# Performance work log

Hardware: AMD Instinct MI355X
Metric: run time of the kernel (lower is better)

The kernel has to match this reference:

```python
import jax, jax.numpy as jnp
import numpy as np

HEADS, DIM_HEAD = 8, 96
DIM = HEADS * DIM_HEAD            # 768
DEPTH = 8
MEM_LAYERS = (4, 5)               # layers with KNN-retrieval attention
TOPK = 32                         # num_retrieved_memories
CLIP_LEN, PREFIX_LEN = 10, 10
NEG = -1e9


def layernorm(x, g, b):
    m = x.mean(-1, keepdims=True)
    v = ((x - m) ** 2).mean(-1, keepdims=True)
    return (x - m) * jax.lax.rsqrt(v + 1e-5) * g + b


def attention(x, wq_l, wkv_l, wo_l, mem_k=None, mem_v=None):
    # one-headed key/values (memorizing-transformers style), multi-head queries
    b, n, _ = x.shape
    q = (x @ wq_l).reshape(b, n, HEADS, DIM_HEAD).transpose(0, 2, 1, 3)  # [b,h,n,d]
    q = q * (DIM_HEAD ** -0.5)
    kv = x @ wkv_l                                   # [b,n,2d]
    k, v = kv[..., :DIM_HEAD], kv[..., DIM_HEAD:]    # [b,n,d] each
    sim = jnp.einsum('bhid,bjd->bhij', q, k)         # local scores
    causal = jnp.tril(jnp.ones((n, n), dtype=bool))
    sim = jnp.where(causal, sim, NEG)
    if mem_k is not None:
        # exact inner-product top-k retrieval from per-batch memory bank
        mem_sim = jnp.einsum('bhid,bmd->bhim', q, mem_k)      # [b,h,n,M]
        top_sim, top_idx = jax.lax.top_k(mem_sim, TOPK)       # [b,h,n,K]
        mem_v_sel = jnp.take_along_axis(
            mem_v[:, None, None], top_idx[..., None], axis=3)  # [b,h,n,K,d]
        attn = jax.nn.softmax(jnp.concatenate([top_sim, sim], axis=-1), axis=-1)
        mem_attn, loc_attn = attn[..., :TOPK], attn[..., TOPK:]
        out = (jnp.einsum('bhij,bhijd->bhid', mem_attn, mem_v_sel)
               + jnp.einsum('bhij,bjd->bhid', loc_attn, v))
    else:
        attn = jax.nn.softmax(sim, axis=-1)
        out = jnp.einsum('bhij,bjd->bhid', attn, v)
    out = out.transpose(0, 2, 1, 3).reshape(b, n, DIM)
    return out @ wo_l


def setup_inputs() -> dict:
    key = jax.random.key(0)
    ks = jax.random.split(key, 12)
    s = 0.02
    inp = {
        'x': jax.random.normal(ks[0], (16, 640), jnp.float32),
        'linear_w': jax.random.normal(ks[1], (640, CLIP_LEN * DIM), jnp.float32) * s,
        'linear_b': jnp.zeros((CLIP_LEN * DIM,), jnp.float32),
        'prefix_const': jax.random.normal(ks[2], (PREFIX_LEN, DIM), jnp.float32),
        'ln1_g': jnp.ones((DEPTH, DIM), jnp.float32),
        'ln1_b': jnp.zeros((DEPTH, DIM), jnp.float32),
        'wq': jax.random.normal(ks[3], (DEPTH, DIM, DIM), jnp.float32) * s,
        'wkv': jax.random.normal(ks[4], (DEPTH, DIM, 2 * DIM_HEAD), jnp.float32) * s,
        'wo': jax.random.normal(ks[5], (DEPTH, DIM, DIM), jnp.float32) * s,
        'ln2_g': jnp.ones((DEPTH, DIM), jnp.float32),
        'ln2_b': jnp.zeros((DEPTH, DIM), jnp.float32),
        'w1': jax.random.normal(ks[6], (DEPTH, DIM, 4 * DIM), jnp.float32) * s,
        'b1': jnp.zeros((DEPTH, 4 * DIM), jnp.float32),
        'w2': jax.random.normal(ks[7], (DEPTH, 4 * DIM, DIM), jnp.float32) * s,
        'b2': jnp.zeros((DEPTH, DIM), jnp.float32),
        'lnf_g': jnp.ones((DIM,), jnp.float32),
        'lnf_b': jnp.zeros((DIM,), jnp.float32),
        'mem_k': jax.random.normal(ks[8], (16, 32768, DIM_HEAD), jnp.float32),
        'mem_v': jax.random.normal(ks[9], (16, 32768, DIM_HEAD), jnp.float32),
    }
    return inp


def reference(x, linear_w, linear_b, prefix_const,
              ln1_g, ln1_b, wq, wkv, wo, ln2_g, ln2_b,
              w1, b1, w2, b2, lnf_g, lnf_b, mem_k, mem_v):
    b = x.shape[0]
    # linear projection of clip feature -> clip_length tokens
    h = (x @ linear_w + linear_b).reshape(b, CLIP_LEN, DIM)
    prefix = jnp.broadcast_to(prefix_const[None], (b, PREFIX_LEN, DIM))
    t = jnp.concatenate([h, prefix], axis=1)  # [b, 20, dim]
    for l in range(DEPTH):
        mk, mv = (mem_k, mem_v) if l in MEM_LAYERS else (None, None)
        t = t + attention(layernorm(t, ln1_g[l], ln1_b[l]), wq[l], wkv[l], wo[l], mk, mv)
        hf = layernorm(t, ln2_g[l], ln2_b[l])
        t = t + (jax.nn.gelu(hf @ w1[l] + b1[l]) @ w2[l] + b2[l])
    t = layernorm(t, lnf_g, lnf_b)
    return t[:, CLIP_LEN:]  # [b, prefix_length, dim]
```

## Files before the change

### kernel.cpp

```cpp
#include <hip/hip_runtime.h>
#include <hip/hip_bf16.h>

#define BB 16
#define NSEQ 20
#define HEADS 8
#define DH 96
#define DIM 768
#define FF 3072
#define KMEM 32768
#define NCHUNK 4
#define CHUNK 8192
#define CAP 128
#define ALDS 776

typedef unsigned short u16;
typedef __attribute__((ext_vector_type(8))) short short8v;
typedef __attribute__((ext_vector_type(4))) float f32x4;

__device__ __forceinline__ u16 f2bu(float x) {
    __hip_bfloat16 h = __float2bfloat16(x);
    return *reinterpret_cast<u16*>(&h);
}

__global__ __launch_bounds__(256) void conv_k(const float* __restrict__ src, u16* __restrict__ dst, int n)
{
    int i = blockIdx.x * 256 + threadIdx.x;
    if (i < n) dst[i] = f2bu(src[i]);
}

__device__ __forceinline__ void tconv_tile(const float* __restrict__ src, u16* __restrict__ dst,
                                           int K, int N, int kt, int nt, int tx, int ty)
{
    __shared__ float tile[32][33];
    int k0 = kt * 32, n0 = nt * 32;
#pragma unroll
    for (int i = 0; i < 4; i++)
        tile[ty + 8 * i][tx] = src[(size_t)(k0 + ty + 8 * i) * N + n0 + tx];
    __syncthreads();
#pragma unroll
    for (int i = 0; i < 4; i++)
        dst[(size_t)(n0 + ty + 8 * i) * K + k0 + tx] = f2bu(tile[tx][ty + 8 * i]);
}

__global__ __launch_bounds__(256) void tconv_k(const float* __restrict__ src, u16* __restrict__ dst, int K, int N)
{
    int tilesN = N >> 5;
    tconv_tile(src, dst, K, N, blockIdx.x / tilesN, blockIdx.x % tilesN,
               threadIdx.x & 31, threadIdx.x >> 5);
}

__global__ __launch_bounds__(256) void wconv5L_k(const float* __restrict__ wq, const float* __restrict__ wkv,
    const float* __restrict__ wo, const float* __restrict__ w1, const float* __restrict__ w2,
    u16* __restrict__ wt, size_t wtStride)
{
    int l = blockIdx.y;
    wq += (size_t)l * 589824;
    wkv += (size_t)l * 147456;
    wo += (size_t)l * 589824;
    w1 += (size_t)l * 2359296;
    w2 += (size_t)l * 2359296;
    wt += (size_t)l * wtStride;
    int bx = blockIdx.x;
    int tx = threadIdx.x & 31, ty = threadIdx.x >> 5;
    if (bx < 576)       tconv_tile(wq,  wt + 0,       768, 768,  bx / 24,          bx % 24,          tx, ty);
    else if (bx < 720)  tconv_tile(wkv, wt + 589824,  768, 192,  (bx - 576) / 6,   (bx - 576) % 6,   tx, ty);
    else if (bx < 1296) tconv_tile(wo,  wt + 737280,  768, 768,  (bx - 720) / 24,  (bx - 720) % 24,  tx, ty);
    else if (bx < 3600) tconv_tile(w1,  wt + 1327104, 768, 3072, (bx - 1296) / 96, (bx - 1296) % 96, tx, ty);
    else                tconv_tile(w2,  wt + 3686400, 3072, 768, (bx - 3600) / 24, (bx - 3600) % 24, tx, ty);
}

__device__ __forceinline__ void storeC(float* C, size_t idx, float v) { C[idx] = v; }
__device__ __forceinline__ void storeC(u16* C, size_t idx, float v)   { C[idx] = f2bu(v); }

template <typename CT>
__global__ __launch_bounds__(256) void gemm_bt(const u16* __restrict__ A, const u16* __restrict__ Bt,
    const float* __restrict__ bias, const float* __restrict__ resid, CT* __restrict__ C,
    int M, int N, int K, int lda, int ldc, float scale, int act)
{
    int tid = threadIdx.x;
    int w = tid >> 6, lane = tid & 63;
    int m0 = blockIdx.y * 16;
    int n0 = blockIdx.x * 128 + w * 32;
    int row = lane & 15;
    int kg  = lane >> 4;
    const u16* arow = A + (size_t)(m0 + row) * lda + kg * 8;
    int c0 = n0 + row;
    int c1 = n0 + 16 + row;
    const u16* bt0 = Bt + (size_t)min(c0, N - 1) * K + kg * 8;
    const u16* bt1 = Bt + (size_t)min(c1, N - 1) * K + kg * 8;
    f32x4 acc0 = {0.f, 0.f, 0.f, 0.f};
    f32x4 acc1 = {0.f, 0.f, 0.f, 0.f};
#pragma unroll 4
    for (int k0 = 0; k0 < K; k0 += 32) {
        short8v af = *(const short8v*)(arow + k0);
        short8v b0 = *(const short8v*)(bt0 + k0);
        short8v b1 = *(const short8v*)(bt1 + k0);
        acc0 = __builtin_amdgcn_mfma_f32_16x16x32_bf16(af, b0, acc0, 0, 0, 0);
        acc1 = __builtin_amdgcn_mfma_f32_16x16x32_bf16(af, b1, acc1, 0, 0, 0);
    }
#pragma unroll
    for (int r = 0; r < 4; r++) {
        int rw = m0 + kg * 4 + r;
        if (c0 < N) {
            float v = acc0[r] * scale;
            if (bias) v += bias[c0];
            if (act) {
                float xx = v;
                float tt = 0.7978845608028654f * (xx + 0.044715f * xx * xx * xx);
                v = 0.5f * xx * (1.0f + tanhf(tt));
            }
            if (resid) v += resid[(size_t)rw * ldc + c0];
            storeC(C, (size_t)rw * ldc + c0, v);
        }
        if (c1 < N) {
            float v = acc1[r] * scale;
            if (bias) v += bias[c1];
            if (act) {
                float xx = v;
                float tt = 0.7978845608028654f * (xx + 0.044715f * xx * xx * xx);
                v = 0.5f * xx * (1.0f + tanhf(tt));
            }
            if (resid) v += resid[(size_t)rw * ldc + c1];
            storeC(C, (size_t)rw * ldc + c1, v);
        }
    }
}

__device__ __forceinline__ void ln_stage(const float* __restrict__ t, const float* __restrict__ g,
    const float* __restrict__ bln, int m0, int tid, u16* __restrict__ As)
{
    int lane = tid & 63, w = tid >> 6;
    int rl = w * 4 + (lane >> 4);
    int sl = lane & 15;
    const float4* tr = (const float4*)(t + (size_t)(m0 + rl) * DIM);
    float4 xv[12];
    float sum = 0.f;
#pragma unroll
    for (int i = 0; i < 12; i++) {
        xv[i] = tr[i * 16 + sl];
        sum += xv[i].x + xv[i].y + xv[i].z + xv[i].w;
    }
    sum += __shfl_xor(sum, 1); sum += __shfl_xor(sum, 2);
    sum += __shfl_xor(sum, 4); sum += __shfl_xor(sum, 8);
    float mean = sum * (1.f / 768.f);
    float vs = 0.f;
#pragma unroll
    for (int i = 0; i < 12; i++) {
        float dx = xv[i].x - mean, dy = xv[i].y - mean;
        float dz = xv[i].z - mean, dw2 = xv[i].w - mean;
        vs += dx * dx + dy * dy + dz * dz + dw2 * dw2;
    }
    vs += __shfl_xor(vs, 1); vs += __shfl_xor(vs, 2);
    vs += __shfl_xor(vs, 4); vs += __shfl_xor(vs, 8);
    float rs = rsqrtf(vs * (1.f / 768.f) + 1e-5f);
    u16* arow = As + (size_t)rl * ALDS;
#pragma unroll
    for (int i = 0; i < 12; i++) {
        int col = i * 64 + sl * 4;
        float4 gv = *(const float4*)(g + col);
        float4 bv = *(const float4*)(bln + col);
        ushort4 ov;
        ov.x = f2bu((xv[i].x - mean) * rs * gv.x + bv.x);
        ov.y = f2bu((xv[i].y - mean) * rs * gv.y + bv.y);
        ov.z = f2bu((xv[i].z - mean) * rs * gv.z + bv.z);
        ov.w = f2bu((xv[i].w - mean) * rs * gv.w + bv.w);
        *(ushort4*)(arow + col) = ov;
    }
}

__global__ __launch_bounds__(256) void gemm_ln_qkv(const float* __restrict__ t,
    const float* __restrict__ g, const float* __restrict__ bln, const u16* __restrict__ Bt,
    float* __restrict__ qb, float* __restrict__ kvb, float qscale)
{
    __shared__ u16 As[16 * ALDS];
    const int N = 960, K = DIM;
    int tid = threadIdx.x;
    int m0 = blockIdx.y * 16;
    ln_stage(t, g, bln, m0, tid, As);
    __syncthreads();
    int w = tid >> 6, lane = tid & 63;
    int n0 = blockIdx.x * 128 + w * 32;
    int row = lane & 15;
    int kg  = lane >> 4;
    const u16* arow = As + (size_t)row * ALDS + kg * 8;
    int c0 = n0 + row;
    int c1 = n0 + 16 + row;
    const u16* bt0 = Bt + (size_t)min(c0, N - 1) * K + kg * 8;
    const u16* bt1 = Bt + (size_t)min(c1, N - 1) * K + kg * 8;
    f32x4 acc0 = {0.f, 0.f, 0.f, 0.f};
    f32x4 acc1 = {0.f, 0.f, 0.f, 0.f};
#pragma unroll 4
    for (int k0 = 0; k0 < K; k0 += 32) {
        short8v af = *(const short8v*)(arow + k0);
        short8v b0 = *(const short8v*)(bt0 + k0);
        short8v b1 = *(const short8v*)(bt1 + k0);
        acc0 = __builtin_amdgcn_mfma_f32_16x16x32_bf16(af, b0, acc0, 0, 0, 0);
        acc1 = __builtin_amdgcn_mfma_f32_16x16x32_bf16(af, b1, acc1, 0, 0, 0);
    }
#pragma unroll
    for (int r = 0; r < 4; r++) {
        int rw = m0 + kg * 4 + r;
        if (c0 < 768)      qb[(size_t)rw * 768 + c0] = acc0[r] * qscale;
        else if (c0 < 960) kvb[(size_t)rw * 192 + (c0 - 768)] = acc0[r];
        if (c1 < 768)      qb[(size_t)rw * 768 + c1] = acc1[r] * qscale;
        else if (c1 < 960) kvb[(size_t)rw * 192 + (c1 - 768)] = acc1[r];
    }
}

__global__ __launch_bounds__(256) void gemm_ln_w1(const float* __restrict__ t,
    const float* __restrict__ g, const float* __restrict__ bln, const u16* __restrict__ Bt,
    const float* __restrict__ bias, u16* __restrict__ C)
{
    __shared__ u16 As[16 * ALDS];
    const int N = FF, K = DIM;
    int tid = threadIdx.x;
    int m0 = blockIdx.y * 16;
    ln_stage(t, g, bln, m0, tid, As);
    __syncthreads();
    int w = tid >> 6, lane = tid & 63;
    int n0 = blockIdx.x * 128 + w * 32;
    int row = lane & 15;
    int kg  = lane >> 4;
    const u16* arow = As + (size_t)row * ALDS + kg * 8;
    int c0 = n0 + row;
    int c1 = n0 + 16 + row;
    const u16* bt0 = Bt + (size_t)c0 * K + kg * 8;
    const u16* bt1 = Bt + (size_t)c1 * K + kg * 8;
    f32x4 acc0 = {0.f, 0.f, 0.f, 0.f};
    f32x4 acc1 = {0.f, 0.f, 0.f, 0.f};
#pragma unroll 4
    for (int k0 = 0; k0 < K; k0 += 32) {
        short8v af = *(const short8v*)(arow + k0);
        short8v b0 = *(const short8v*)(bt0 + k0);
        short8v b1 = *(const short8v*)(bt1 + k0);
        acc0 = __builtin_amdgcn_mfma_f32_16x16x32_bf16(af, b0, acc0, 0, 0, 0);
        acc1 = __builtin_amdgcn_mfma_f32_16x16x32_bf16(af, b1, acc1, 0, 0, 0);
    }
#pragma unroll
    for (int r = 0; r < 4; r++) {
        int rw = m0 + kg * 4 + r;
        {
            float v = acc0[r] + bias[c0];
            float tt = 0.7978845608028654f * (v + 0.044715f * v * v * v);
            v = 0.5f * v * (1.0f + tanhf(tt));
            C[(size_t)rw * FF + c0] = f2bu(v);
        }
        {
            float v = acc1[r] + bias[c1];
            float tt = 0.7978845608028654f * (v + 0.044715f * v * v * v);
            v = 0.5f * v * (1.0f + tanhf(tt));
            C[(size_t)rw * FF + c1] = f2bu(v);
        }
    }
}

__global__ __launch_bounds__(256) void lnf_k(const float* __restrict__ x, const float* __restrict__ g,
    const float* __restrict__ bb, float* __restrict__ out)
{
    int blk = blockIdx.x;
    int b = blk / 10, ii = blk - b * 10;
    int row = b * NSEQ + 10 + ii;
    const float* xr = x + (size_t)row * DIM;
    int tid = threadIdx.x;
    float v0 = xr[tid], v1 = xr[tid + 256], v2 = xr[tid + 512];
    __shared__ float red[4];
    float s = v0 + v1 + v2;
    for (int off = 32; off; off >>= 1) s += __shfl_down(s, off);
    if ((tid & 63) == 0) red[tid >> 6] = s;
    __syncthreads();
    float mean = (red[0] + red[1] + red[2] + red[3]) * (1.f / 768.f);
    __syncthreads();
    float d0 = v0 - mean, d1 = v1 - mean, d2 = v2 - mean;
    s = d0 * d0 + d1 * d1 + d2 * d2;
    for (int off = 32; off; off >>= 1) s += __shfl_down(s, off);
    if ((tid & 63) == 0) red[tid >> 6] = s;
    __syncthreads();
    float var = (red[0] + red[1] + red[2] + red[3]) * (1.f / 768.f);
    float rs = rsqrtf(var + 1e-5f);
    float* orow = out + ((size_t)(b * 10 + ii)) * DIM;
    orow[tid]       = d0 * rs * g[tid]       + bb[tid];
    orow[tid + 256] = d1 * rs * g[tid + 256] + bb[tid + 256];
    orow[tid + 512] = d2 * rs * g[tid + 512] + bb[tid + 512];
}

__global__ __launch_bounds__(256) void prefix_k(const float* __restrict__ p, float* __restrict__ t)
{
    int idx = blockIdx.x * 256 + threadIdx.x;
    if (idx < BB * 7680) {
        int b = idx / 7680;
        int r = idx - b * 7680;
        t[(size_t)b * (NSEQ * DIM) + 7680 + r] = p[r];
    }
}

__device__ __forceinline__ float dot96(const float* __restrict__ a, const float* __restrict__ b)
{
    float s = 0.f;
#pragma unroll
    for (int d4 = 0; d4 < 24; d4++) {
        float4 av = *(const float4*)(a + d4 * 4);
        float4 bv = *(const float4*)(b + d4 * 4);
        s = fmaf(av.x, bv.x, s);
        s = fmaf(av.y, bv.y, s);
        s = fmaf(av.z, bv.z, s);
        s = fmaf(av.w, bv.w, s);
    }
    return s;
}

__global__ __launch_bounds__(256) void lattn_k(const float* __restrict__ q, const float* __restrict__ kv,
    u16* __restrict__ ao)
{
    int b = blockIdx.x, h = blockIdx.y;
    __shared__ float sims[NSEQ][NSEQ];
    __shared__ float probs[NSEQ][NSEQ];
    const float* qb = q + (size_t)b * NSEQ * DIM + h * DH;
    const float* kb = kv + (size_t)b * NSEQ * 192;
    int tid = threadIdx.x;
    for (int p = tid; p < NSEQ * NSEQ; p += 256) {
        int i = p / NSEQ, j = p - i * NSEQ;
        float s;
        if (j > i) s = -1.0e9f;
        else s = dot96(qb + (size_t)i * DIM, kb + j * 192);
        sims[i][j] = s;
    }
    __syncthreads();
    if (tid < NSEQ) {
        int i = tid;
        float m = -1e30f;
        for (int j = 0; j < NSEQ; j++) m = fmaxf(m, sims[i][j]);
        float sum = 0.f;
        for (int j = 0; j < NSEQ; j++) { float e = expf(sims[i][j] - m); probs[i][j] = e; sum += e; }
        float inv = 1.f / sum;
        for (int j = 0; j < NSEQ; j++) probs[i][j] *= inv;
    }
    __syncthreads();
    for (int p = tid; p < NSEQ * DH; p += 256) {
        int i = p / DH, d = p - i * DH;
        float o = 0.f;
        for (int j = 0; j <= i; j++) o = fmaf(probs[i][j], kb[j * 192 + 96 + d], o);
        ao[((size_t)b * NSEQ + i) * DIM + h * DH + d] = f2bu(o);
    }
}

__device__ __forceinline__ bool tk_better(float va, int ia, float vb, int ib) {
    return (va > vb) || (va == vb && ia < ib);
}

__device__ __forceinline__ void lds_fence() {
    asm volatile("s_waitcnt lgkmcnt(0)" ::: "memory");
    __builtin_amdgcn_sched_barrier(0);
}

__device__ void topk32(float* bv, int* bi, int cnt, int lane,
                       float& ov, int& oi, float& thr_out) {
    lds_fence();
    float v0 = (lane < cnt)      ? bv[lane]      : -3.0e38f;
    int   i0 = (lane < cnt)      ? bi[lane]      : 0x7fffffff;
    float v1 = (lane + 64 < cnt) ? bv[lane + 64] : -3.0e38f;
    int   i1 = (lane + 64 < cnt) ? bi[lane + 64] : 0x7fffffff;
    lds_fence();
#pragma unroll
    for (int k = 2; k <= 128; k <<= 1) {
#pragma unroll
        for (int j = 64; j >= 1; j >>= 1) {
            if (j >= k) continue;
            if (j == 64) {
                bool asc = ((lane & k) == 0);
                bool b01 = tk_better(v0, i0, v1, i1);
                if (b01 != asc) { float tv = v0; int ti = i0; v0 = v1; i0 = i1; v1 = tv; i1 = ti; }
            } else {
                {
                    float pv = __shfl_xor(v0, j); int pi = __shfl_xor(i0, j);
                    bool asc = ((lane & k) == 0);
                    bool first = ((lane & j) == 0);
                    bool mb = tk_better(v0, i0, pv, pi);
                    bool keep = first ? (mb == asc) : (mb != asc);
                    if (!keep) { v0 = pv; i0 = pi; }
                }
                {
                    float pv = __shfl_xor(v1, j); int pi = __shfl_xor(i1, j);
                    bool asc = (((lane + 64) & k) == 0);
                    bool first = ((lane & j) == 0);
                    bool mb = tk_better(v1, i1, pv, pi);
                    bool keep = first ? (mb == asc) : (mb != asc);
                    if (!keep) { v1 = pv; i1 = pi; }
                }
            }
        }
    }
    if (lane < 32) { bv[lane] = v0; bi[lane] = i0; }
    lds_fence();
    ov = v0; oi = i0;
    thr_out = __shfl(v0, 31);
}

__device__ __forceinline__ void tk_pass(const float4 kr[6], const float4 qreg[5][6],
    float thrR[5], int cntR[5], float (*bufv)[CAP], int (*bufi)[CAP],
    int r0, int lane, int qt, int key)
{
    float a[5];
#pragma unroll
    for (int rr = 0; rr < 5; rr++) a[rr] = 0.f;
#pragma unroll
    for (int i = 0; i < 6; i++) {
        float4 kv = kr[i];
#pragma unroll
        for (int rr = 0; rr < 5; rr++) {
            float4 qv = qreg[rr][i];
            a[rr] = fmaf(qv.x, kv.x, a[rr]);
            a[rr] = fmaf(qv.y, kv.y, a[rr]);
            a[rr] = fmaf(qv.z, kv.z, a[rr]);
            a[rr] = fmaf(qv.w, kv.w, a[rr]);
        }
    }
#pragma unroll
    for (int rr = 0; rr < 5; rr++) {
        a[rr] += __shfl_xor(a[rr], 1);
        a[rr] += __shfl_xor(a[rr], 2);
    }
    unsigned long long m[5];
#pragma unroll
    for (int rr = 0; rr < 5; rr++) {
        bool cand = (qt == 0) && (a[rr] >= thrR[rr]);
        m[rr] = __ballot(cand);
    }
    if (m[0] | m[1] | m[2] | m[3] | m[4]) {
#pragma unroll
        for (int rr = 0; rr < 5; rr++) {
            if (m[rr]) {
                int n = __popcll(m[rr]);
                int r = r0 + rr;
                if (cntR[rr] + n > CAP) {
                    float dv; int di;
                    topk32(&bufv[r][0], &bufi[r][0], cntR[rr], lane, dv, di, thrR[rr]);
                    cntR[rr] = 32;
                }
                int pos = cntR[rr] + __popcll(m[rr] & ((1ull << lane) - 1ull));
                if ((m[rr] >> lane) & 1ull) { bufv[r][pos] = a[rr]; bufi[r][pos] = key; }
                cntR[rr] += n;
            }
        }
    }
}

__global__ __launch_bounds__(256) __attribute__((amdgpu_waves_per_eu(2, 2)))
void memtopk_k(const float* __restrict__ q, const float* __restrict__ memk,
    float* __restrict__ tkv, int* __restrict__ tki)
{
    __shared__ float bufv[NSEQ][CAP];
    __shared__ int   bufi[NSEQ][CAP];
    int c = blockIdx.x, h = blockIdx.y, b = blockIdx.z;
    int tid = threadIdx.x;
    int lane = tid & 63;
    int w = tid >> 6;
    int r0 = w * 5;
    int qt = lane & 3;
    int kk = lane >> 2;

    float4 qreg[5][6];
#pragma unroll
    for (int rr = 0; rr < 5; rr++) {
        const float4* qrow = (const float4*)(q + ((size_t)(b * NSEQ + r0 + rr)) * DIM + h * DH + qt * 24);
#pragma unroll
        for (int i = 0; i < 6; i++) qreg[rr][i] = qrow[i];
    }

    float thrR[5]; int cntR[5];
#pragma unroll
    for (int rr = 0; rr < 5; rr++) { thrR[rr] = -3.0e38f; cntR[rr] = 0; }

    const char* kbase = (const char*)(memk + (size_t)b * KMEM * DH);
    int k0 = c * CHUNK;
    unsigned off = ((unsigned)(k0 + kk) * 96u + (unsigned)qt * 24u) * 4u;
    const unsigned TILE = 16u * 96u * 4u;

    float4 kA[12], kB[12];
#pragma unroll
    for (int s = 0; s < 2; s++)
#pragma unroll
        for (int i = 0; i < 6; i++)
            kA[s * 6 + i] = *(const float4*)(kbase + (off + s * TILE + i * 16u));
    for (int p = 0; p < CHUNK / 16; p += 4) {
        int key0 = k0 + p * 16 + kk;
#pragma unroll
        for (int s = 0; s < 2; s++)
#pragma unroll
            for (int i = 0; i < 6; i++)
                kB[s * 6 + i] = *(const float4*)(kbase + (off + (2u + s) * TILE + i * 16u));
        tk_pass(kA + 0, qreg, thrR, cntR, bufv, bufi, r0, lane, qt, key0);
        tk_pass(kA + 6, qreg, thrR, cntR, bufv, bufi, r0, lane, qt, key0 + 16);
        if (p + 4 < CHUNK / 16) {
#pragma unroll
            for (int s = 0; s < 2; s++)
#pragma unroll
                for (int i = 0; i < 6; i++)
                    kA[s * 6 + i] = *(const float4*)(kbase + (off + (4u + s) * TILE + i * 16u));
        }
        tk_pass(kB + 0, qreg, thrR, cntR, bufv, bufi, r0, lane, qt, key0 + 32);
        tk_pass(kB + 6, qreg, thrR, cntR, bufv, bufi, r0, lane, qt, key0 + 48);
        off += 4u * TILE;
    }
#pragma unroll
    for (int rr = 0; rr < 5; rr++) {
        int r = r0 + rr;
        float ov; int oi; float dthr;
        topk32(&bufv[r][0], &bufi[r][0], cntR[rr], lane, ov, oi, dthr);
        if (lane < 32) {
            size_t base = ((((size_t)b * HEADS + h) * NSEQ + r) * NCHUNK + c) * 32;
            tkv[base + lane] = ov;
            tki[base + lane] = oi;
        }
    }
}

__global__ __launch_bounds__(64) void memattn_k(const float* __restrict__ q, const float* __restrict__ kv,
    const float* __restrict__ memv, const float* __restrict__ tkv, const int* __restrict__ tki,
    u16* __restrict__ ao)
{
    int i = blockIdx.x, h = blockIdx.y, b = blockIdx.z;
    __shared__ float cv[NCHUNK * 32];
    __shared__ int   ci[NCHUNK * 32];
    __shared__ float selv[32];
    __shared__ int   seli[32];
    __shared__ float ls[NSEQ];
    __shared__ float probs[52];
    int tid = threadIdx.x;
    size_t base = (((size_t)b * HEADS + h) * NSEQ + i) * (NCHUNK * 32);
#pragma unroll
    for (int s = 0; s < NCHUNK * 32 / 64; s++) {
        cv[tid + 64 * s] = tkv[base + tid + 64 * s];
        ci[tid + 64 * s] = tki[base + tid + 64 * s];
    }
    const float* qr = q + ((size_t)b * NSEQ + i) * DIM + h * DH;
    const float* kvb = kv + (size_t)b * NSEQ * 192;
    if (tid <= i) {
        float s = dot96(qr, kvb + tid * 192);
        ls[tid] = s;
    }
    __syncthreads();
    for (int r = 0; r < 32; r++) {
        float bv = -3.0e38f; int bidx = 0x7fffffff; int bs = 0;
#pragma unroll
        for (int s = 0; s < NCHUNK * 32 / 64; s++) {
            float v = cv[tid + 64 * s]; int ix = ci[tid + 64 * s];
            if (tk_better(v, ix, bv, bidx)) { bv = v; bidx = ix; bs = tid + 64 * s; }
        }
        for (int off = 32; off; off >>= 1) {
            float ovv = __shfl_down(bv, off);
            int oii = __shfl_down(bidx, off);
            int oss = __shfl_down(bs, off);
            if (tk_better(ovv, oii, bv, bidx)) { bv = ovv; bidx = oii; bs = oss; }
        }
        if (tid == 0) { selv[r] = bv; seli[r] = bidx; cv[bs] = -3.0e38f; }
        __syncthreads();
    }
    if (tid == 0) {
        float m = -1e30f;
        for (int r = 0; r < 32; r++) m = fmaxf(m, selv[r]);
        for (int j = 0; j <= i; j++) m = fmaxf(m, ls[j]);
        float sum = 0.f;
        for (int r = 0; r < 32; r++) { float e = expf(selv[r] - m); probs[r] = e; sum += e; }
        for (int j = 0; j <= i; j++) { float e = expf(ls[j] - m); probs[32 + j] = e; sum += e; }
        float inv = 1.f / sum;
        for (int r = 0; r < 32 + i + 1; r++) probs[r] *= inv;
    }
    __syncthreads();
    const float* mvb = memv + (size_t)b * KMEM * DH;
    for (int d = tid; d < DH; d += 64) {
        float o = 0.f;
        for (int r = 0; r < 32; r++) o = fmaf(probs[r], mvb[(size_t)seli[r] * DH + d], o);
        for (int j = 0; j <= i; j++) o = fmaf(probs[32 + j], kvb[j * 192 + 96 + d], o);
        ao[((size_t)b * NSEQ + i) * DIM + h * DH + d] = f2bu(o);
    }
}

extern "C" void kernel_launch(void* const* d_in, const int* in_sizes, int n_in,
                              void* d_out, int out_size, void* d_ws, size_t ws_size,
                              hipStream_t stream) {
    const float* x            = (const float*)d_in[0];
    const float* linear_w     = (const float*)d_in[1];
    const float* linear_b     = (const float*)d_in[2];
    const float* prefix_const = (const float*)d_in[3];
    const float* ln1_g        = (const float*)d_in[4];
    const float* ln1_b        = (const float*)d_in[5];
    const float* wq           = (const float*)d_in[6];
    const float* wkv          = (const float*)d_in[7];
    const float* wo           = (const float*)d_in[8];
    const float* ln2_g        = (const float*)d_in[9];
    const float* ln2_b        = (const float*)d_in[10];
    const float* w1           = (const float*)d_in[11];
    const float* b1           = (const float*)d_in[12];
    const float* w2           = (const float*)d_in[13];
    const float* b2           = (const float*)d_in[14];
    const float* lnf_g        = (const float*)d_in[15];
    const float* lnf_b        = (const float*)d_in[16];
    const float* mem_k        = (const float*)d_in[17];
    const float* mem_v        = (const float*)d_in[18];

    float* ws = (float*)d_ws;
    float* t    = ws;
    float* qb   = ws + 491520;
    float* kvb  = ws + 737280;
    u16*   aob  = (u16*)(ws + 798720);
    u16*   h1b  = (u16*)(ws + 1044480);
    float* tkv  = ws + 2027520;
    int*   tki  = (int*)(ws + 2355200);
    u16*   wt   = (u16*)(ws + 2682880);
    float* out  = (float*)d_out;

    const size_t LAYER_WT = 6045696;
    const int all8 = (ws_size >= (size_t)(2682880 + 8 * 3022848 + 2560) * 4) ? 1 : 0;
    u16* xb = (u16*)(ws + (all8 ? (2682880 + 8 * 3022848) : (2682880 + 3022848)));

    const float qscale = 0.10206207261596577f;
    const size_t WOT = 737280, W1T = 1327104, W2T = 3686400;

    conv_k<<<40, 256, 0, stream>>>(x, xb, 16 * 640);
    tconv_k<<<4800, 256, 0, stream>>>(linear_w, wt, 640, 7680);
    gemm_bt<float><<<dim3(60, 1), 256, 0, stream>>>(xb, wt, linear_b, nullptr, t,
                                                    16, 7680, 640, 640, 15360, 1.f, 0);
    prefix_k<<<dim3(480), 256, 0, stream>>>(prefix_const, t);

    if (all8)
        wconv5L_k<<<dim3(5904, 8), 256, 0, stream>>>(wq, wkv, wo, w1, w2, wt, LAYER_WT);

    for (int l = 0; l < 8; l++) {
        u16* wtl = wt + (all8 ? (size_t)l * LAYER_WT : 0);
        if (!all8)
            wconv5L_k<<<dim3(5904, 1), 256, 0, stream>>>(wq + (size_t)l * 589824, wkv + (size_t)l * 147456,
                                                         wo + (size_t)l * 589824, w1 + (size_t)l * 2359296,
                                                         w2 + (size_t)l * 2359296, wtl, 0);
        gemm_ln_qkv<<<dim3(8, 20), 256, 0, stream>>>(t, ln1_g + (size_t)l * DIM, ln1_b + (size_t)l * DIM,
                                                     wtl, qb, kvb, qscale);
        if (l == 4 || l == 5) {
            memtopk_k<<<dim3(NCHUNK, HEADS, BB), 256, 0, stream>>>(qb, mem_k, tkv, tki);
            memattn_k<<<dim3(NSEQ, HEADS, BB), 64, 0, stream>>>(qb, kvb, mem_v, tkv, tki, aob);
        } else {
            lattn_k<<<dim3(BB, HEADS), 256, 0, stream>>>(qb, kvb, aob);
        }
        gemm_bt<float><<<dim3(6, 20), 256, 0, stream>>>(aob, wtl + WOT, nullptr, t, t,
                                                        320, 768, 768, 768, 768, 1.f, 0);
        gemm_ln_w1<<<dim3(24, 20), 256, 0, stream>>>(t, ln2_g + (size_t)l * DIM, ln2_b + (size_t)l * DIM,
                                                     wtl + W1T, b1 + (size_t)l * FF, h1b);
        gemm_bt<float><<<dim3(6, 20), 256, 0, stream>>>(h1b, wtl + W2T, b2 + (size_t)l * DIM, t, t,
                                                        320, 768, 3072, 3072, 768, 1.f, 0);
    }
    lnf_k<<<160, 256, 0, stream>>>(t, lnf_g, lnf_b, out);
}
```

Before: 1.974 ms.

## Split memory top-k rows across eight waves and drop manual key prefetch

The memory top-k kernel now launches 512 threads per block (8 waves) instead of 256, with the first four waves handling 3 query rows each and the last four handling 2 rows each, instead of 4 waves of 5 rows. The explicit double-buffered key register prefetch is replaced by a simple per-tile load loop. The aim is more waves per block to hide memory latency and fewer registers per thread. The trade-off is that each key tile is now loaded by 8 waves instead of 4, doubling L2/global traffic for the mem_k stream, and the kernel loses its software pipelining.

```diff
diff --git a/kernel.cpp b/kernel.cpp
--- a/kernel.cpp
+++ b/kernel.cpp
@@ -395,18 +395,19 @@
     thr_out = __shfl(v0, 31);
 }
 
-__device__ __forceinline__ void tk_pass(const float4 kr[6], const float4 qreg[5][6],
-    float thrR[5], int cntR[5], float (*bufv)[CAP], int (*bufi)[CAP],
+template <int NR>
+__device__ __forceinline__ void tk_passN(const float4 kr[6], const float4 (*qreg)[6],
+    float* thrR, int* cntR, float (*bufv)[CAP], int (*bufi)[CAP],
     int r0, int lane, int qt, int key)
 {
-    float a[5];
-#pragma unroll
-    for (int rr = 0; rr < 5; rr++) a[rr] = 0.f;
+    float a[NR];
+#pragma unroll
+    for (int rr = 0; rr < NR; rr++) a[rr] = 0.f;
 #pragma unroll
     for (int i = 0; i < 6; i++) {
         float4 kv = kr[i];
 #pragma unroll
-        for (int rr = 0; rr < 5; rr++) {
+        for (int rr = 0; rr < NR; rr++) {
             float4 qv = qreg[rr][i];
             a[rr] = fmaf(qv.x, kv.x, a[rr]);
             a[rr] = fmaf(qv.y, kv.y, a[rr]);
@@ -415,19 +416,21 @@
         }
     }
 #pragma unroll
-    for (int rr = 0; rr < 5; rr++) {
+    for (int rr = 0; rr < NR; rr++) {
         a[rr] += __shfl_xor(a[rr], 1);
         a[rr] += __shfl_xor(a[rr], 2);
     }
-    unsigned long long m[5];
-#pragma unroll
-    for (int rr = 0; rr < 5; rr++) {
+    unsigned long long m[NR];
+    unsigned long long any = 0ull;
+#pragma unroll
+    for (int rr = 0; rr < NR; rr++) {
         bool cand = (qt == 0) && (a[rr] >= thrR[rr]);
         m[rr] = __ballot(cand);
-    }
-    if (m[0] | m[1] | m[2] | m[3] | m[4]) {
-#pragma unroll
-        for (int rr = 0; rr < 5; rr++) {
+        any |= m[rr];
+    }
+    if (any) {
+#pragma unroll
+        for (int rr = 0; rr < NR; rr++) {
             if (m[rr]) {
                 int n = __popcll(m[rr]);
                 int r = r0 + rr;
@@ -444,65 +447,35 @@
     }
 }
 
-__global__ __launch_bounds__(256) __attribute__((amdgpu_waves_per_eu(2, 2)))
-void memtopk_k(const float* __restrict__ q, const float* __restrict__ memk,
-    float* __restrict__ tkv, int* __restrict__ tki)
-{
-    __shared__ float bufv[NSEQ][CAP];
-    __shared__ int   bufi[NSEQ][CAP];
-    int c = blockIdx.x, h = blockIdx.y, b = blockIdx.z;
-    int tid = threadIdx.x;
-    int lane = tid & 63;
-    int w = tid >> 6;
-    int r0 = w * 5;
-    int qt = lane & 3;
-    int kk = lane >> 2;
-
-    float4 qreg[5][6];
-#pragma unroll
-    for (int rr = 0; rr < 5; rr++) {
+template <int NR>
+__device__ void topk_run(const float* __restrict__ q, const char* __restrict__ kbase,
+    float (*bufv)[CAP], int (*bufi)[CAP], float* __restrict__ tkv, int* __restrict__ tki,
+    int b, int h, int c, int r0, int lane, int qt, int kk, int k0, unsigned off0)
+{
+    float4 qreg[NR][6];
+#pragma unroll
+    for (int rr = 0; rr < NR; rr++) {
         const float4* qrow = (const float4*)(q + ((size_t)(b * NSEQ + r0 + rr)) * DIM + h * DH + qt * 24);
 #pragma unroll
         for (int i = 0; i < 6; i++) qreg[rr][i] = qrow[i];
     }
-
-    float thrR[5]; int cntR[5];
-#pragma unroll
-    for (int rr = 0; rr < 5; rr++) { thrR[rr] = -3.0e38f; cntR[rr] = 0; }
-
-    const char* kbase = (const char*)(memk + (size_t)b * KMEM * DH);
-    int k0 = c * CHUNK;
-    unsigned off = ((unsigned)(k0 + kk) * 96u + (unsigned)qt * 24u) * 4u;
+    float thrR[NR]; int cntR[NR];
+#pragma unroll
+    for (int rr = 0; rr < NR; rr++) { thrR[rr] = -3.0e38f; cntR[rr] = 0; }
+
     const unsigned TILE = 16u * 96u * 4u;
-
-    float4 kA[12], kB[12];
-#pragma unroll
-    for (int s = 0; s < 2; s++)
+    unsigned off = off0;
+    for (int p = 0; p < CHUNK / 16; p++) {
+        int key0 = k0 + p * 16 + kk;
+        float4 kA[6];
 #pragma unroll
         for (int i = 0; i < 6; i++)
-            kA[s * 6 + i] = *(const float4*)(kbase + (off + s * TILE + i * 16u));
-    for (int p = 0; p < CHUNK / 16; p += 4) {
-        int key0 = k0 + p * 16 + kk;
-#pragma unroll
-        for (int s = 0; s < 2; s++)
-#pragma unroll
-            for (int i = 0; i < 6; i++)
-                kB[s * 6 + i] = *(const float4*)(kbase + (off + (2u + s) * TILE + i * 16u));
-        tk_pass(kA + 0, qreg, thrR, cntR, bufv, bufi, r0, lane, qt, key0);
-        tk_pass(kA + 6, qreg, thrR, cntR, bufv, bufi, r0, lane, qt, key0 + 16);
-        if (p + 4 < CHUNK / 16) {
-#pragma unroll
-            for (int s = 0; s < 2; s++)
-#pragma unroll
-                for (int i = 0; i < 6; i++)
-                    kA[s * 6 + i] = *(const float4*)(kbase + (off + (4u + s) * TILE + i * 16u));
-        }
-        tk_pass(kB + 0, qreg, thrR, cntR, bufv, bufi, r0, lane, qt, key0 + 32);
-        tk_pass(kB + 6, qreg, thrR, cntR, bufv, bufi, r0, lane, qt, key0 + 48);
-        off += 4u * TILE;
-    }
-#pragma unroll
-    for (int rr = 0; rr < 5; rr++) {
+            kA[i] = *(const float4*)(kbase + (off + i * 16u));
+        tk_passN<NR>(kA, qreg, thrR, cntR, bufv, bufi, r0, lane, qt, key0);
+        off += TILE;
+    }
+#pragma unroll
+    for (int rr = 0; rr < NR; rr++) {
         int r = r0 + rr;
         float ov; int oi; float dthr;
         topk32(&bufv[r][0], &bufi[r][0], cntR[rr], lane, ov, oi, dthr);
@@ -512,6 +485,29 @@
             tki[base + lane] = oi;
         }
     }
+}
+
+__global__ __launch_bounds__(512, 4)
+void memtopk_k(const float* __restrict__ q, const float* __restrict__ memk,
+    float* __restrict__ tkv, int* __restrict__ tki)
+{
+    __shared__ float bufv[NSEQ][CAP];
+    __shared__ int   bufi[NSEQ][CAP];
+    int c = blockIdx.x, h = blockIdx.y, b = blockIdx.z;
+    int tid = threadIdx.x;
+    int lane = tid & 63;
+    int w = tid >> 6;
+    int qt = lane & 3;
+    int kk = lane >> 2;
+
+    const char* kbase = (const char*)(memk + (size_t)b * KMEM * DH);
+    int k0 = c * CHUNK;
+    unsigned off0 = ((unsigned)(k0 + kk) * 96u + (unsigned)qt * 24u) * 4u;
+
+    if (w < 4)
+        topk_run<3>(q, kbase, bufv, bufi, tkv, tki, b, h, c, w * 3, lane, qt, kk, k0, off0);
+    else
+        topk_run<2>(q, kbase, bufv, bufi, tkv, tki, b, h, c, 12 + (w - 4) * 2, lane, qt, kk, k0, off0);
 }
 
 __global__ __launch_bounds__(64) void memattn_k(const float* __restrict__ q, const float* __restrict__ kv,
@@ -634,7 +630,7 @@
         gemm_ln_qkv<<<dim3(8, 20), 256, 0, stream>>>(t, ln1_g + (size_t)l * DIM, ln1_b + (size_t)l * DIM,
                                                      wtl, qb, kvb, qscale);
         if (l == 4 || l == 5) {
-            memtopk_k<<<dim3(NCHUNK, HEADS, BB), 256, 0, stream>>>(qb, mem_k, tkv, tki);
+            memtopk_k<<<dim3(NCHUNK, HEADS, BB), 512, 0, stream>>>(qb, mem_k, tkv, tki);
             memattn_k<<<dim3(NSEQ, HEADS, BB), 64, 0, stream>>>(qb, kvb, mem_v, tkv, tki, aob);
         } else {
             lattn_k<<<dim3(BB, HEADS), 256, 0, stream>>>(qb, kvb, aob);
```

Measured after the change: 2.614 ms. +32.4%, slower.
